# Kernel optimization log

Measured on AMD Instinct MI355X. Metric: run time of the kernel, lower is better.

The kernel has to match this reference:

```python
import jax, jax.numpy as jnp
import numpy as np

T, B, DIM, N = 2, 256, 512, 196


def setup_inputs() -> dict:
    key = jax.random.key(0)
    ks = jax.random.split(key, 6)
    scale_mem = (2.0 / (DIM + DIM)) ** 0.5      # GlorotNormal
    scale_cat = (2.0 / (2 * DIM + DIM)) ** 0.5
    scale_attn = (2.0 / (DIM + 1)) ** 0.5
    return {
        "memory": jax.random.normal(ks[0], (T, B, DIM), dtype=jnp.float32),
        "know": jax.random.normal(ks[1], (B, DIM, N), dtype=jnp.float32),
        "control": jax.random.normal(ks[2], (T, B, DIM), dtype=jnp.float32),
        "W_mem": jax.random.normal(ks[3], (DIM, DIM), dtype=jnp.float32) * scale_mem,
        "b_mem": jnp.zeros((DIM,), dtype=jnp.float32),
        "W_concat": jax.random.normal(ks[4], (2 * DIM, DIM), dtype=jnp.float32) * scale_cat,
        "b_concat": jnp.zeros((DIM,), dtype=jnp.float32),
        "W_attn": jax.random.normal(ks[5], (DIM, 1), dtype=jnp.float32) * scale_attn,
        "b_attn": jnp.zeros((1,), dtype=jnp.float32),
    }


def reference(memory, know, control, W_mem, b_mem, W_concat, b_concat, W_attn, b_attn):
    # mem = Dense(dim)(memory[-1]) -> [B, dim]
    mem = memory[-1] @ W_mem + b_mem
    # mem[..., None] * know -> [B, dim, N]; concat along channel axis -> [B, 2*dim, N]
    cat = jnp.concatenate([mem[:, :, None] * know, know], axis=1)
    # transpose to [B, N, 2*dim], Dense(dim) -> [B, N, dim]
    concat = jnp.swapaxes(cat, 1, 2) @ W_concat + b_concat
    # gate by control[-1] -> [B, N, dim]; Dense(1) + squeeze -> [B, N]
    attn = concat * control[-1][:, None, :]
    logits = jnp.squeeze(attn @ W_attn, -1) + b_attn[0]
    # softmax over N, then (faithfully) weighted sum over the dim axis -> [B, N]
    a = jax.nn.softmax(logits, axis=1)[:, None, :]  # [B, 1, N]
    read = jnp.sum(a * know, axis=1)  # [B, N]
    return read
```

## Files before the change

kernel.cpp:

```cpp
#include <hip/hip_runtime.h>
#include <cfloat>

#define BB   256
#define DIM  512
#define NN   196
#define BT   8
#define IT   32

__global__ __launch_bounds__(512, 4) void prep_kernel(
    const float* __restrict__ memory,
    const float* __restrict__ control,
    const float* __restrict__ W_mem,
    const float* __restrict__ b_mem,
    const float* __restrict__ W_concat,
    const float* __restrict__ W_attn,
    float* __restrict__ w_out)
{
    __shared__ float4 MU4[4][DIM];
    __shared__ float  buf[12288];

    const int tid = threadIdx.x;
    const int il  = tid & 31;
    const int kg  = tid >> 5;
    const int b0  = blockIdx.x * BT;
    const int i0  = blockIdx.y * IT;

    const float* mem_in = memory  + (size_t)BB * DIM;
    const float* ctl_in = control + (size_t)BB * DIM;

    {
        const float wa = W_attn[tid];
        #pragma unroll
        for (int p = 0; p < 4; ++p) {
            MU4[p][tid] = make_float4(
                mem_in[(size_t)(b0 + 2 * p)     * DIM + tid],
                ctl_in[(size_t)(b0 + 2 * p)     * DIM + tid] * wa,
                mem_in[(size_t)(b0 + 2 * p + 1) * DIM + tid],
                ctl_in[(size_t)(b0 + 2 * p + 1) * DIM + tid] * wa);
        }
    }

    float am[8] = {0,0,0,0,0,0,0,0};
    float a1[8] = {0,0,0,0,0,0,0,0};
    float a2[8] = {0,0,0,0,0,0,0,0};

    const int sr = tid >> 4;
    const int sc = tid & 15;
    float2* WT = (float2*)buf;

    float4 f1 = *(const float4*)&W_concat[(size_t)(i0 + sr) * DIM + sc * 4];
    float4 f2 = *(const float4*)&W_concat[(size_t)(DIM + i0 + sr) * DIM + sc * 4];
    float wmc[4], wmn[4];
    #pragma unroll
    for (int j = 0; j < 4; ++j)
        wmc[j] = W_mem[(size_t)(kg * 4 + j) * DIM + i0 + il];

    for (int kt = 0; kt < DIM; kt += 64) {
        __syncthreads();

        {
            const float* f1f = (const float*)&f1;
            const float* f2f = (const float*)&f2;
            #pragma unroll
            for (int j = 0; j < 4; ++j)
                WT[(sc * 4 + j) * 33 + sr] = make_float2(f1f[j], f2f[j]);
        }
        if (kt + 64 < DIM) {
            f1 = *(const float4*)&W_concat[(size_t)(i0 + sr) * DIM + kt + 64 + sc * 4];
            f2 = *(const float4*)&W_concat[(size_t)(DIM + i0 + sr) * DIM + kt + 64 + sc * 4];
        }
        __syncthreads();

        if (kt + 64 < DIM) {
            #pragma unroll
            for (int j = 0; j < 4; ++j)
                wmn[j] = W_mem[(size_t)(kt + 64 + kg * 4 + j) * DIM + i0 + il];
        }

        #pragma unroll
        for (int j = 0; j < 4; ++j) {
            const int kl = kg * 4 + j;
            const int k  = kt + kl;
            const float2 c = WT[kl * 33 + il];
            #pragma unroll
            for (int p = 0; p < 4; ++p) {
                const float4 mu = MU4[p][k];
                am[2 * p]     = fmaf(mu.x, wmc[j], am[2 * p]);
                a1[2 * p]     = fmaf(mu.y, c.x,    a1[2 * p]);
                a2[2 * p]     = fmaf(mu.y, c.y,    a2[2 * p]);
                am[2 * p + 1] = fmaf(mu.z, wmc[j], am[2 * p + 1]);
                a1[2 * p + 1] = fmaf(mu.w, c.x,    a1[2 * p + 1]);
                a2[2 * p + 1] = fmaf(mu.w, c.y,    a2[2 * p + 1]);
            }
        }
        #pragma unroll
        for (int j = 0; j < 4; ++j) wmc[j] = wmn[j];
    }

    __syncthreads();
    #pragma unroll
    for (int b = 0; b < 8; ++b) {
        const int row = (kg * 8 + b) * 32 + il;
        buf[row]        = am[b];
        buf[4096 + row] = a1[b];
        buf[8192 + row] = a2[b];
    }
    __syncthreads();
    if (tid < 256) {
        const int rb = tid >> 5, ri = tid & 31;
        float sm = 0.f, s1 = 0.f, s2 = 0.f;
        #pragma unroll
        for (int t = 0; t < 16; ++t) {
            const int row = (t * 8 + rb) * 32 + ri;
            sm += buf[row];
            s1 += buf[4096 + row];
            s2 += buf[8192 + row];
        }
        w_out[(size_t)(b0 + rb) * DIM + i0 + ri] =
            (sm + b_mem[i0 + ri]) * s1 + s2;
    }
}

__global__ __launch_bounds__(1024) void read_kernel(
    const float* __restrict__ know,
    const float* __restrict__ w,
    float* __restrict__ out)
{
    __shared__ float  w_s[DIM];
    __shared__ float4 part_lg[16][50];
    __shared__ float4 part_ks[16][50];
    __shared__ float  tmp[256];
    __shared__ float  bc[2];

    const int tx  = threadIdx.x;
    const int ty  = threadIdx.y;
    const int tid = ty * 64 + tx;
    const int b   = blockIdx.x;

    if (tid < DIM) w_s[tid] = w[(size_t)b * DIM + tid];
    __syncthreads();

    float4 lg = make_float4(0.f, 0.f, 0.f, 0.f);
    float4 ks = make_float4(0.f, 0.f, 0.f, 0.f);
    if (tx < 49) {
        const float4* kp = (const float4*)(know + (size_t)b * DIM * NN) + (size_t)(ty * 32) * 49 + tx;
        const float*  wp = w_s + ty * 32;
        #pragma unroll 8
        for (int dd = 0; dd < 32; ++dd) {
            const float4 kv = kp[(size_t)dd * 49];
            const float  wv = wp[dd];
            lg.x = fmaf(kv.x, wv, lg.x); lg.y = fmaf(kv.y, wv, lg.y);
            lg.z = fmaf(kv.z, wv, lg.z); lg.w = fmaf(kv.w, wv, lg.w);
            ks.x += kv.x; ks.y += kv.y; ks.z += kv.z; ks.w += kv.w;
        }
        part_lg[ty][tx] = lg;
        part_ks[ty][tx] = ks;
    }
    __syncthreads();

    float lgn = 0.f, ksn = 0.f;
    if (tid < NN) {
        const int ng = tid >> 2, j = tid & 3;
        #pragma unroll
        for (int t = 0; t < 16; ++t) {
            lgn += ((const float*)&part_lg[t][ng])[j];
            ksn += ((const float*)&part_ks[t][ng])[j];
        }
    }

    if (tid < 256) tmp[tid] = (tid < NN) ? lgn : -FLT_MAX;
    __syncthreads();
    if (tid < 64) {
        float m = fmaxf(fmaxf(tmp[tid], tmp[tid + 64]),
                        fmaxf(tmp[tid + 128], tmp[tid + 192]));
        #pragma unroll
        for (int o = 32; o; o >>= 1) m = fmaxf(m, __shfl_down(m, o));
        if (tid == 0) bc[0] = m;
    }
    __syncthreads();

    const float e = (tid < NN) ? __expf(lgn - bc[0]) : 0.f;
    if (tid < 256) tmp[tid] = e;
    __syncthreads();
    if (tid < 64) {
        float s = tmp[tid] + tmp[tid + 64] + tmp[tid + 128] + tmp[tid + 192];
        #pragma unroll
        for (int o = 32; o; o >>= 1) s += __shfl_down(s, o);
        if (tid == 0) bc[1] = s;
    }
    __syncthreads();

    if (tid < NN) out[(size_t)b * NN + tid] = e / bc[1] * ksn;
}

extern "C" void kernel_launch(void* const* d_in, const int* in_sizes, int n_in,
                              void* d_out, int out_size, void* d_ws, size_t ws_size,
                              hipStream_t stream) {
    const float* memory   = (const float*)d_in[0];
    const float* know     = (const float*)d_in[1];
    const float* control  = (const float*)d_in[2];
    const float* W_mem    = (const float*)d_in[3];
    const float* b_mem    = (const float*)d_in[4];
    const float* W_concat = (const float*)d_in[5];
    const float* W_attn   = (const float*)d_in[7];
    float* w_ws = (float*)d_ws;
    float* outp = (float*)d_out;

    prep_kernel<<<dim3(BB / BT, DIM / IT), dim3(512), 0, stream>>>(
        memory, control, W_mem, b_mem, W_concat, W_attn, w_ws);
    read_kernel<<<dim3(BB), dim3(64, 16), 0, stream>>>(know, w_ws, outp);
}
```

Baseline: 36.53 us.

## Widen prep kernel output tile to 64 columns for more register reuse

The prep kernel now computes 64 output columns per block instead of 32. Each thread keeps two sets of accumulators, so every shared-memory load of the memory/control values feeds twice as many FMAs. The grid is halved and launch bounds drop to 2 blocks per SM. Shared memory is merged into one buffer and the final cross-thread reduction is done in three passes to fit it, which adds extra barriers and lowers occupancy.

```diff
diff --git a/kernel.cpp b/kernel.cpp
--- a/kernel.cpp
+++ b/kernel.cpp
@@ -5,9 +5,9 @@
 #define DIM  512
 #define NN   196
 #define BT   8
-#define IT   32
-
-__global__ __launch_bounds__(512, 4) void prep_kernel(
+#define IT   64
+
+__global__ __launch_bounds__(512, 2) void prep_kernel(
     const float* __restrict__ memory,
     const float* __restrict__ control,
     const float* __restrict__ W_mem,
@@ -16,8 +16,9 @@
     const float* __restrict__ W_attn,
     float* __restrict__ w_out)
 {
-    __shared__ float4 MU4[4][DIM];
-    __shared__ float  buf[12288];
+    __shared__ float lds[16768];
+    float4* MU = (float4*)lds;
+    float2* WT = (float2*)(lds + 8192);
 
     const int tid = threadIdx.x;
     const int il  = tid & 31;
@@ -32,7 +33,7 @@
         const float wa = W_attn[tid];
         #pragma unroll
         for (int p = 0; p < 4; ++p) {
-            MU4[p][tid] = make_float4(
+            MU[p * 512 + tid] = make_float4(
                 mem_in[(size_t)(b0 + 2 * p)     * DIM + tid],
                 ctl_in[(size_t)(b0 + 2 * p)     * DIM + tid] * wa,
                 mem_in[(size_t)(b0 + 2 * p + 1) * DIM + tid],
@@ -40,85 +41,127 @@
         }
     }
 
-    float am[8] = {0,0,0,0,0,0,0,0};
-    float a1[8] = {0,0,0,0,0,0,0,0};
-    float a2[8] = {0,0,0,0,0,0,0,0};
-
     const int sr = tid >> 4;
     const int sc = tid & 15;
-    float2* WT = (float2*)buf;
-
-    float4 f1 = *(const float4*)&W_concat[(size_t)(i0 + sr) * DIM + sc * 4];
-    float4 f2 = *(const float4*)&W_concat[(size_t)(DIM + i0 + sr) * DIM + sc * 4];
-    float wmc[4], wmn[4];
-    #pragma unroll
-    for (int j = 0; j < 4; ++j)
-        wmc[j] = W_mem[(size_t)(kg * 4 + j) * DIM + i0 + il];
+    const float* w1l = W_concat + (size_t)(i0 + sr)            * DIM;
+    const float* w2l = W_concat + (size_t)(DIM + i0 + sr)      * DIM;
+    const float* w1h = W_concat + (size_t)(i0 + 32 + sr)       * DIM;
+    const float* w2h = W_concat + (size_t)(DIM + i0 + 32 + sr) * DIM;
+
+    float4 f1l = *(const float4*)(w1l + sc * 4);
+    float4 f2l = *(const float4*)(w2l + sc * 4);
+    float4 f1h = *(const float4*)(w1h + sc * 4);
+    float4 f2h = *(const float4*)(w2h + sc * 4);
+
+    float wmc[4][2], wmn[4][2];
+    #pragma unroll
+    for (int j = 0; j < 4; ++j) {
+        wmc[j][0] = W_mem[(size_t)(kg * 4 + j) * DIM + i0 + il];
+        wmc[j][1] = W_mem[(size_t)(kg * 4 + j) * DIM + i0 + 32 + il];
+    }
+
+    float am[8][2] = {}, a1[8][2] = {}, a2[8][2] = {};
 
     for (int kt = 0; kt < DIM; kt += 64) {
         __syncthreads();
 
         {
-            const float* f1f = (const float*)&f1;
-            const float* f2f = (const float*)&f2;
+            const float* pa = (const float*)&f1l;
+            const float* pb = (const float*)&f2l;
+            const float* pc = (const float*)&f1h;
+            const float* pd = (const float*)&f2h;
             #pragma unroll
-            for (int j = 0; j < 4; ++j)
-                WT[(sc * 4 + j) * 33 + sr] = make_float2(f1f[j], f2f[j]);
+            for (int cc = 0; cc < 4; ++cc) {
+                const int k = sc * 4 + cc;
+                WT[k * 67 + sr]      = make_float2(pa[cc], pb[cc]);
+                WT[k * 67 + 32 + sr] = make_float2(pc[cc], pd[cc]);
+            }
         }
         if (kt + 64 < DIM) {
-            f1 = *(const float4*)&W_concat[(size_t)(i0 + sr) * DIM + kt + 64 + sc * 4];
-            f2 = *(const float4*)&W_concat[(size_t)(DIM + i0 + sr) * DIM + kt + 64 + sc * 4];
+            f1l = *(const float4*)(w1l + kt + 64 + sc * 4);
+            f2l = *(const float4*)(w2l + kt + 64 + sc * 4);
+            f1h = *(const float4*)(w1h + kt + 64 + sc * 4);
+            f2h = *(const float4*)(w2h + kt + 64 + sc * 4);
         }
         __syncthreads();
 
         if (kt + 64 < DIM) {
             #pragma unroll
-            for (int j = 0; j < 4; ++j)
-                wmn[j] = W_mem[(size_t)(kt + 64 + kg * 4 + j) * DIM + i0 + il];
+            for (int j = 0; j < 4; ++j) {
+                wmn[j][0] = W_mem[(size_t)(kt + 64 + kg * 4 + j) * DIM + i0 + il];
+                wmn[j][1] = W_mem[(size_t)(kt + 64 + kg * 4 + j) * DIM + i0 + 32 + il];
+            }
         }
 
         #pragma unroll
         for (int j = 0; j < 4; ++j) {
             const int kl = kg * 4 + j;
             const int k  = kt + kl;
-            const float2 c = WT[kl * 33 + il];
+            const float2 cl = WT[kl * 67 + il];
+            const float2 ch = WT[kl * 67 + 32 + il];
             #pragma unroll
             for (int p = 0; p < 4; ++p) {
-                const float4 mu = MU4[p][k];
-                am[2 * p]     = fmaf(mu.x, wmc[j], am[2 * p]);
-                a1[2 * p]     = fmaf(mu.y, c.x,    a1[2 * p]);
-                a2[2 * p]     = fmaf(mu.y, c.y,    a2[2 * p]);
-                am[2 * p + 1] = fmaf(mu.z, wmc[j], am[2 * p + 1]);
-                a1[2 * p + 1] = fmaf(mu.w, c.x,    a1[2 * p + 1]);
-                a2[2 * p + 1] = fmaf(mu.w, c.y,    a2[2 * p + 1]);
+                const float4 mu = MU[p * 512 + k];
+                am[2*p][0]   = fmaf(mu.x, wmc[j][0], am[2*p][0]);
+                am[2*p][1]   = fmaf(mu.x, wmc[j][1], am[2*p][1]);
+                a1[2*p][0]   = fmaf(mu.y, cl.x, a1[2*p][0]);
+                a1[2*p][1]   = fmaf(mu.y, ch.x, a1[2*p][1]);
+                a2[2*p][0]   = fmaf(mu.y, cl.y, a2[2*p][0]);
+                a2[2*p][1]   = fmaf(mu.y, ch.y, a2[2*p][1]);
+                am[2*p+1][0] = fmaf(mu.z, wmc[j][0], am[2*p+1][0]);
+                am[2*p+1][1] = fmaf(mu.z, wmc[j][1], am[2*p+1][1]);
+                a1[2*p+1][0] = fmaf(mu.w, cl.x, a1[2*p+1][0]);
+                a1[2*p+1][1] = fmaf(mu.w, ch.x, a1[2*p+1][1]);
+                a2[2*p+1][0] = fmaf(mu.w, cl.y, a2[2*p+1][0]);
+                a2[2*p+1][1] = fmaf(mu.w, ch.y, a2[2*p+1][1]);
             }
         }
         #pragma unroll
-        for (int j = 0; j < 4; ++j) wmc[j] = wmn[j];
-    }
+        for (int j = 0; j < 4; ++j) {
+            wmc[j][0] = wmn[j][0];
+            wmc[j][1] = wmn[j][1];
+        }
+    }
+
+    const int rb  = tid >> 6;
+    const int ilo = tid & 63;
+    float sm, s1v, s2v;
 
     __syncthreads();
     #pragma unroll
     for (int b = 0; b < 8; ++b) {
-        const int row = (kg * 8 + b) * 32 + il;
-        buf[row]        = am[b];
-        buf[4096 + row] = a1[b];
-        buf[8192 + row] = a2[b];
-    }
-    __syncthreads();
-    if (tid < 256) {
-        const int rb = tid >> 5, ri = tid & 31;
-        float sm = 0.f, s1 = 0.f, s2 = 0.f;
-        #pragma unroll
-        for (int t = 0; t < 16; ++t) {
-            const int row = (t * 8 + rb) * 32 + ri;
-            sm += buf[row];
-            s1 += buf[4096 + row];
-            s2 += buf[8192 + row];
-        }
-        w_out[(size_t)(b0 + rb) * DIM + i0 + ri] =
-            (sm + b_mem[i0 + ri]) * s1 + s2;
-    }
+        lds[(kg * 8 + b) * 64 + il]      = am[b][0];
+        lds[(kg * 8 + b) * 64 + 32 + il] = am[b][1];
+    }
+    __syncthreads();
+    sm = 0.f;
+    #pragma unroll
+    for (int t = 0; t < 16; ++t) sm += lds[(t * 8 + rb) * 64 + ilo];
+
+    __syncthreads();
+    #pragma unroll
+    for (int b = 0; b < 8; ++b) {
+        lds[(kg * 8 + b) * 64 + il]      = a1[b][0];
+        lds[(kg * 8 + b) * 64 + 32 + il] = a1[b][1];
+    }
+    __syncthreads();
+    s1v = 0.f;
+    #pragma unroll
+    for (int t = 0; t < 16; ++t) s1v += lds[(t * 8 + rb) * 64 + ilo];
+
+    __syncthreads();
+    #pragma unroll
+    for (int b = 0; b < 8; ++b) {
+        lds[(kg * 8 + b) * 64 + il]      = a2[b][0];
+        lds[(kg * 8 + b) * 64 + 32 + il] = a2[b][1];
+    }
+    __syncthreads();
+    s2v = 0.f;
+    #pragma unroll
+    for (int t = 0; t < 16; ++t) s2v += lds[(t * 8 + rb) * 64 + ilo];
+
+    w_out[(size_t)(b0 + rb) * DIM + i0 + ilo] =
+        (sm + b_mem[i0 + ilo]) * s1v + s2v;
 }
 
 __global__ __launch_bounds__(1024) void read_kernel(
```

After: 36.70 us. Within noise of the previous version (+0.5%).

## Run prep GEMMs on bf16 MFMA with a separate conversion kernel

Applied to the files above, without the earlier changes.

Adds a conversion kernel that casts W_concat, a transposed W_mem, memory and the W_attn-scaled control rows to bf16 in workspace. A new prep kernel then computes the three small GEMMs with 16x16x32 bf16 MFMA instructions instead of scalar FP32 FMAs. This is meant to cut the FP32 FMA cost of the prep stage. In exchange it adds a kernel launch, an extra round trip through global memory and bf16 rounding error, and it keeps the old path as a fallback when the workspace is too small.

```diff
diff --git a/kernel.cpp b/kernel.cpp
--- a/kernel.cpp
+++ b/kernel.cpp
@@ -4,16 +4,144 @@
 #define BB   256
 #define DIM  512
 #define NN   196
-#define BT   8
-#define IT   32
-
-__global__ __launch_bounds__(512, 4) void prep_kernel(
-    const float* __restrict__ memory,
-    const float* __restrict__ control,
-    const float* __restrict__ W_mem,
+
+typedef __attribute__((ext_vector_type(8))) short bf16x8;
+typedef __attribute__((ext_vector_type(4))) float f32x4;
+
+__device__ __forceinline__ ushort f2bf(float x) {
+    unsigned u = __float_as_uint(x);
+    return (ushort)((u + 0x7FFFu + ((u >> 16) & 1u)) >> 16);
+}
+
+__global__ __launch_bounds__(256) void convert_kernel(
+    const float* __restrict__ memory, const float* __restrict__ control,
+    const float* __restrict__ W_mem, const float* __restrict__ W_concat,
+    const float* __restrict__ W_attn,
+    ushort* __restrict__ Wt,
+    ushort* __restrict__ mu)
+{
+    const int tid = threadIdx.x;
+    const int blk = blockIdx.x;
+
+    if (blk < 128) {
+        const float4* in4 = (const float4*)W_concat;
+        uint2* out = (uint2*)(Wt + (size_t)DIM * DIM);
+        #pragma unroll
+        for (int p = 0; p < 4; ++p) {
+            const int idx = blk * 1024 + p * 256 + tid;
+            const float4 q = in4[idx];
+            uint2 o;
+            o.x = (unsigned)f2bf(q.x) | ((unsigned)f2bf(q.y) << 16);
+            o.y = (unsigned)f2bf(q.z) | ((unsigned)f2bf(q.w) << 16);
+            out[idx] = o;
+        }
+    } else if (blk < 192) {
+        __shared__ float T[64][65];
+        const int t  = blk - 128;
+        const int tk = (t >> 3) * 64, ti = (t & 7) * 64;
+        const int r  = tid >> 2;
+        const int cb = (tid & 3) * 16;
+        #pragma unroll
+        for (int j = 0; j < 16; j += 4) {
+            const float4 q = *(const float4*)&W_mem[(size_t)(tk + r) * DIM + ti + cb + j];
+            T[r][cb + j + 0] = q.x; T[r][cb + j + 1] = q.y;
+            T[r][cb + j + 2] = q.z; T[r][cb + j + 3] = q.w;
+        }
+        __syncthreads();
+        const int ii = tid & 63;
+        const int kq = tid >> 6;
+        #pragma unroll
+        for (int kk = 0; kk < 16; kk += 2) {
+            const int k = kq * 16 + kk;
+            const unsigned v = (unsigned)f2bf(T[k][ii]) | ((unsigned)f2bf(T[k + 1][ii]) << 16);
+            *(unsigned*)&Wt[(size_t)(ti + ii) * DIM + tk + k] = v;
+        }
+    } else {
+        const float4* mem4 = (const float4*)(memory  + (size_t)BB * DIM);
+        const float4* ctl4 = (const float4*)(control + (size_t)BB * DIM);
+        const float4* wa4  = (const float4*)W_attn;
+        uint2* out = (uint2*)mu;
+        #pragma unroll
+        for (int p = 0; p < 4; ++p) {
+            const int idx = (blk - 192) * 1024 + p * 256 + tid;
+            const int sec = idx >> 15;
+            const int j   = idx & 32767;
+            float4 q = sec ? ctl4[j] : mem4[j];
+            if (sec) {
+                const float4 wa = wa4[j & 127];
+                q.x *= wa.x; q.y *= wa.y; q.z *= wa.z; q.w *= wa.w;
+            }
+            uint2 o;
+            o.x = (unsigned)f2bf(q.x) | ((unsigned)f2bf(q.y) << 16);
+            o.y = (unsigned)f2bf(q.z) | ((unsigned)f2bf(q.w) << 16);
+            out[(size_t)sec * 32768 + j] = o;
+        }
+    }
+}
+
+__global__ __launch_bounds__(128) void prep_mfma(
+    const ushort* __restrict__ Wt,
+    const ushort* __restrict__ mu,
     const float* __restrict__ b_mem,
-    const float* __restrict__ W_concat,
-    const float* __restrict__ W_attn,
+    float* __restrict__ w_out)
+{
+    __shared__ __align__(16) ushort mus[2][16][520];
+
+    const int tid = threadIdx.x;
+    const int wv  = tid >> 6;
+    const int l   = tid & 63;
+    const int b0  = blockIdx.x * 16;
+    const int i0  = blockIdx.y * 32;
+
+    #pragma unroll
+    for (int p = 0; p < 16; ++p) {
+        const int idx = p * 128 + tid;
+        const int a   = idx >> 10;
+        const int rb  = (idx >> 6) & 15;
+        const int kc  = (idx & 63) * 8;
+        *(uint4*)&mus[a][rb][kc] =
+            *(const uint4*)&mu[((size_t)a * BB + b0 + rb) * DIM + kc];
+    }
+    __syncthreads();
+
+    const int fr = l & 15;
+    const int fk = (l >> 4) * 8;
+
+    f32x4 accM = {0.f, 0.f, 0.f, 0.f};
+    f32x4 acc1 = {0.f, 0.f, 0.f, 0.f};
+    f32x4 acc2 = {0.f, 0.f, 0.f, 0.f};
+
+    const int ib = i0 + wv * 16 + fr;
+    const ushort* wm = Wt + ((size_t)0 * DIM + ib) * DIM;
+    const ushort* c1 = Wt + ((size_t)1 * DIM + ib) * DIM;
+    const ushort* c2 = Wt + ((size_t)2 * DIM + ib) * DIM;
+
+    #pragma unroll 4
+    for (int t = 0; t < 16; ++t) {
+        const int k = t * 32 + fk;
+        const bf16x8 am = *(const bf16x8*)&mus[0][fr][k];
+        const bf16x8 au = *(const bf16x8*)&mus[1][fr][k];
+        const bf16x8 bm = *(const bf16x8*)&wm[k];
+        const bf16x8 b1 = *(const bf16x8*)&c1[k];
+        const bf16x8 b2 = *(const bf16x8*)&c2[k];
+        accM = __builtin_amdgcn_mfma_f32_16x16x32_bf16(am, bm, accM, 0, 0, 0);
+        acc1 = __builtin_amdgcn_mfma_f32_16x16x32_bf16(au, b1, acc1, 0, 0, 0);
+        acc2 = __builtin_amdgcn_mfma_f32_16x16x32_bf16(au, b2, acc2, 0, 0, 0);
+    }
+
+    const float bmv = b_mem[ib];
+    const int rb0 = (l >> 4) * 4;
+    #pragma unroll
+    for (int r = 0; r < 4; ++r) {
+        w_out[(size_t)(b0 + rb0 + r) * DIM + ib] =
+            (accM[r] + bmv) * acc1[r] + acc2[r];
+    }
+}
+
+__global__ __launch_bounds__(512, 4) void prep_fallback(
+    const float* __restrict__ memory, const float* __restrict__ control,
+    const float* __restrict__ W_mem, const float* __restrict__ b_mem,
+    const float* __restrict__ W_concat, const float* __restrict__ W_attn,
     float* __restrict__ w_out)
 {
     __shared__ float4 MU4[4][DIM];
@@ -22,8 +150,8 @@
     const int tid = threadIdx.x;
     const int il  = tid & 31;
     const int kg  = tid >> 5;
-    const int b0  = blockIdx.x * BT;
-    const int i0  = blockIdx.y * IT;
+    const int b0  = blockIdx.x * 8;
+    const int i0  = blockIdx.y * 32;
 
     const float* mem_in = memory  + (size_t)BB * DIM;
     const float* ctl_in = control + (size_t)BB * DIM;
@@ -40,10 +168,7 @@
         }
     }
 
-    float am[8] = {0,0,0,0,0,0,0,0};
-    float a1[8] = {0,0,0,0,0,0,0,0};
-    float a2[8] = {0,0,0,0,0,0,0,0};
-
+    float am[8] = {}, a1[8] = {}, a2[8] = {};
     const int sr = tid >> 4;
     const int sc = tid & 15;
     float2* WT = (float2*)buf;
@@ -57,7 +182,6 @@
 
     for (int kt = 0; kt < DIM; kt += 64) {
         __syncthreads();
-
         {
             const float* f1f = (const float*)&f1;
             const float* f2f = (const float*)&f2;
@@ -70,13 +194,11 @@
             f2 = *(const float4*)&W_concat[(size_t)(DIM + i0 + sr) * DIM + kt + 64 + sc * 4];
         }
         __syncthreads();
-
         if (kt + 64 < DIM) {
             #pragma unroll
             for (int j = 0; j < 4; ++j)
                 wmn[j] = W_mem[(size_t)(kt + 64 + kg * 4 + j) * DIM + i0 + il];
         }
-
         #pragma unroll
         for (int j = 0; j < 4; ++j) {
             const int kl = kg * 4 + j;
@@ -84,13 +206,13 @@
             const float2 c = WT[kl * 33 + il];
             #pragma unroll
             for (int p = 0; p < 4; ++p) {
-                const float4 mu = MU4[p][k];
-                am[2 * p]     = fmaf(mu.x, wmc[j], am[2 * p]);
-                a1[2 * p]     = fmaf(mu.y, c.x,    a1[2 * p]);
-                a2[2 * p]     = fmaf(mu.y, c.y,    a2[2 * p]);
-                am[2 * p + 1] = fmaf(mu.z, wmc[j], am[2 * p + 1]);
-                a1[2 * p + 1] = fmaf(mu.w, c.x,    a1[2 * p + 1]);
-                a2[2 * p + 1] = fmaf(mu.w, c.y,    a2[2 * p + 1]);
+                const float4 muv = MU4[p][k];
+                am[2*p]   = fmaf(muv.x, wmc[j], am[2*p]);
+                a1[2*p]   = fmaf(muv.y, c.x,    a1[2*p]);
+                a2[2*p]   = fmaf(muv.y, c.y,    a2[2*p]);
+                am[2*p+1] = fmaf(muv.z, wmc[j], am[2*p+1]);
+                a1[2*p+1] = fmaf(muv.w, c.x,    a1[2*p+1]);
+                a2[2*p+1] = fmaf(muv.w, c.y,    a2[2*p+1]);
             }
         }
         #pragma unroll
@@ -203,10 +325,24 @@
     const float* b_mem    = (const float*)d_in[4];
     const float* W_concat = (const float*)d_in[5];
     const float* W_attn   = (const float*)d_in[7];
+    float* outp = (float*)d_out;
+
+    const size_t W_BYTES  = (size_t)BB * DIM * sizeof(float);
+    const size_t WT_BYTES = (size_t)3 * DIM * DIM * sizeof(ushort);
+    const size_t MU_BYTES = (size_t)2 * BB * DIM * sizeof(ushort);
+
     float* w_ws = (float*)d_ws;
-    float* outp = (float*)d_out;
-
-    prep_kernel<<<dim3(BB / BT, DIM / IT), dim3(512), 0, stream>>>(
-        memory, control, W_mem, b_mem, W_concat, W_attn, w_ws);
+
+    if (ws_size >= W_BYTES + WT_BYTES + MU_BYTES) {
+        ushort* Wt = (ushort*)((char*)d_ws + W_BYTES);
+        ushort* mu = (ushort*)((char*)d_ws + W_BYTES + WT_BYTES);
+        convert_kernel<<<dim3(256), dim3(256), 0, stream>>>(
+            memory, control, W_mem, W_concat, W_attn, Wt, mu);
+        prep_mfma<<<dim3(BB / 16, DIM / 32), dim3(128), 0, stream>>>(
+            Wt, mu, b_mem, w_ws);
+    } else {
+        prep_fallback<<<dim3(BB / 8, DIM / 32), dim3(512), 0, stream>>>(
+            memory, control, W_mem, b_mem, W_concat, W_attn, w_ws);
+    }
     read_kernel<<<dim3(BB), dim3(64, 16), 0, stream>>>(know, w_ws, outp);
 }
```

After: 33.12 us. -9.3%, faster.

## Fuse prep and read into one cooperative kernel with bf16 MFMA projections

Applied to the files above, without the earlier changes.

Replaces the two-kernel pipeline with a single cooperative-launch kernel. The first phase computes the per-batch weight vector using bf16 MFMA instructions over 256 blocks, then a grid-wide sync is followed by the softmax-weighted read phase. This removes a kernel launch boundary and moves the small GEMMs onto matrix cores, at the cost of bf16 rounding of the inputs and weights and the overhead of a grid barrier. A fallback to the old two-kernel path runs if the cooperative launch fails.

```diff
diff --git a/kernel.cpp b/kernel.cpp
--- a/kernel.cpp
+++ b/kernel.cpp
@@ -1,19 +1,204 @@
 #include <hip/hip_runtime.h>
+#include <hip/hip_cooperative_groups.h>
 #include <cfloat>
+
+namespace cg = cooperative_groups;
 
 #define BB   256
 #define DIM  512
 #define NN   196
-#define BT   8
-#define IT   32
-
-__global__ __launch_bounds__(512, 4) void prep_kernel(
+
+typedef __attribute__((ext_vector_type(8))) short bf16x8;
+typedef __attribute__((ext_vector_type(4))) float f32x4;
+
+__device__ __forceinline__ ushort f2bf(float x) {
+    unsigned u = __float_as_uint(x);
+    return (ushort)((u + 0x7FFFu + ((u >> 16) & 1u)) >> 16);
+}
+
+__device__ __forceinline__ bf16x8 pack8(float4 a, float4 b) {
+    union { bf16x8 v; ushort u[8]; } r;
+    r.u[0] = f2bf(a.x); r.u[1] = f2bf(a.y); r.u[2] = f2bf(a.z); r.u[3] = f2bf(a.w);
+    r.u[4] = f2bf(b.x); r.u[5] = f2bf(b.y); r.u[6] = f2bf(b.z); r.u[7] = f2bf(b.w);
+    return r.v;
+}
+
+__global__ __launch_bounds__(1024) void fused_kernel(
     const float* __restrict__ memory,
     const float* __restrict__ control,
     const float* __restrict__ W_mem,
     const float* __restrict__ b_mem,
     const float* __restrict__ W_concat,
     const float* __restrict__ W_attn,
+    const float* __restrict__ know,
+    float* __restrict__ w_ws,
+    float* __restrict__ out)
+{
+    __shared__ __align__(16) unsigned char smem[49152];
+
+    const int tid = threadIdx.x;
+    const int blk = blockIdx.x;
+
+    {
+        const int b0 = (blk & 15) * 16;
+        const int i0 = (blk >> 4) * 32;
+        ushort (*mus)[16][520] = (ushort (*)[16][520])smem;
+
+        const float* mem_in = memory  + (size_t)BB * DIM;
+        const float* ctl_in = control + (size_t)BB * DIM;
+
+        #pragma unroll
+        for (int p = 0; p < 4; ++p) {
+            const int idx = p * 1024 + tid;
+            const int a   = idx >> 11;
+            const int rb  = (idx >> 7) & 15;
+            const int k4  = idx & 127;
+            const float* src = a ? ctl_in : mem_in;
+            float4 q = *(const float4*)&src[(size_t)(b0 + rb) * DIM + k4 * 4];
+            if (a) {
+                const float4 wa = ((const float4*)W_attn)[k4];
+                q.x *= wa.x; q.y *= wa.y; q.z *= wa.z; q.w *= wa.w;
+            }
+            uint2 o;
+            o.x = (unsigned)f2bf(q.x) | ((unsigned)f2bf(q.y) << 16);
+            o.y = (unsigned)f2bf(q.z) | ((unsigned)f2bf(q.w) << 16);
+            *(uint2*)&mus[a][rb][k4 * 4] = o;
+        }
+        __syncthreads();
+
+        const int wv = tid >> 6;
+        const int l  = tid & 63;
+        const int s  = wv & 1;
+        const int c  = wv >> 1;
+        const int fr = l & 15;
+        const int fk = (l >> 4) * 8;
+        const int ib = i0 + s * 16 + fr;
+
+        f32x4 accM = {0.f,0.f,0.f,0.f}, acc1 = {0.f,0.f,0.f,0.f}, acc2 = {0.f,0.f,0.f,0.f};
+        const float* wmp = W_mem + ib;
+        const float* c1p = W_concat + (size_t)ib * DIM;
+        const float* c2p = W_concat + (size_t)(DIM + ib) * DIM;
+
+        #pragma unroll
+        for (int ts = 0; ts < 2; ++ts) {
+            const int k = c * 64 + ts * 32 + fk;
+            const bf16x8 am = *(const bf16x8*)&mus[0][fr][k];
+            const bf16x8 au = *(const bf16x8*)&mus[1][fr][k];
+            float wmv[8];
+            #pragma unroll
+            for (int j = 0; j < 8; ++j) wmv[j] = wmp[(size_t)(k + j) * DIM];
+            union { bf16x8 v; ushort u[8]; } bm;
+            #pragma unroll
+            for (int j = 0; j < 8; ++j) bm.u[j] = f2bf(wmv[j]);
+            const bf16x8 b1 = pack8(*(const float4*)&c1p[k], *(const float4*)&c1p[k + 4]);
+            const bf16x8 b2 = pack8(*(const float4*)&c2p[k], *(const float4*)&c2p[k + 4]);
+            accM = __builtin_amdgcn_mfma_f32_16x16x32_bf16(am, bm.v, accM, 0, 0, 0);
+            acc1 = __builtin_amdgcn_mfma_f32_16x16x32_bf16(au, b1,   acc1, 0, 0, 0);
+            acc2 = __builtin_amdgcn_mfma_f32_16x16x32_bf16(au, b2,   acc2, 0, 0, 0);
+        }
+
+        __syncthreads();
+        float* P = (float*)smem;
+        const int rb0 = (l >> 4) * 4;
+        #pragma unroll
+        for (int r = 0; r < 4; ++r) {
+            const int idx = (rb0 + r) * 16 + fr;
+            P[           wv * 256 + idx] = accM[r];
+            P[4096     + wv * 256 + idx] = acc1[r];
+            P[8192     + wv * 256 + idx] = acc2[r];
+        }
+        __syncthreads();
+        if (tid < 512) {
+            const int s2 = tid >> 8, idx = tid & 255;
+            float sm = 0.f, v1 = 0.f, v2 = 0.f;
+            #pragma unroll
+            for (int cc = 0; cc < 8; ++cc) {
+                const int w2 = cc * 2 + s2;
+                sm += P[       w2 * 256 + idx];
+                v1 += P[4096 + w2 * 256 + idx];
+                v2 += P[8192 + w2 * 256 + idx];
+            }
+            const int b = b0 + (idx >> 4);
+            const int i = i0 + s2 * 16 + (idx & 15);
+            w_ws[(size_t)b * DIM + i] = (sm + b_mem[i]) * v1 + v2;
+        }
+    }
+
+    __threadfence();
+    cg::this_grid().sync();
+
+    {
+        const int tx = tid & 63;
+        const int ty = tid >> 6;
+        const int b  = blk;
+        float*  w_s     = (float*)smem;
+        float4* part_lg = (float4*)(smem + 2048);
+        float4* part_ks = (float4*)(smem + 2048 + 12800);
+        float*  tmp     = (float*)(smem + 2048 + 25600);
+        float*  bc      = (float*)(smem + 2048 + 25600 + 1024);
+
+        if (tid < DIM) w_s[tid] = w_ws[(size_t)b * DIM + tid];
+        __syncthreads();
+
+        float4 lg = make_float4(0.f, 0.f, 0.f, 0.f);
+        float4 ks = make_float4(0.f, 0.f, 0.f, 0.f);
+        if (tx < 49) {
+            const float4* kp = (const float4*)(know + (size_t)b * DIM * NN)
+                             + (size_t)(ty * 32) * 49 + tx;
+            const float* wp = w_s + ty * 32;
+            #pragma unroll 8
+            for (int dd = 0; dd < 32; ++dd) {
+                const float4 kv = kp[(size_t)dd * 49];
+                const float  wv = wp[dd];
+                lg.x = fmaf(kv.x, wv, lg.x); lg.y = fmaf(kv.y, wv, lg.y);
+                lg.z = fmaf(kv.z, wv, lg.z); lg.w = fmaf(kv.w, wv, lg.w);
+                ks.x += kv.x; ks.y += kv.y; ks.z += kv.z; ks.w += kv.w;
+            }
+            part_lg[ty * 50 + tx] = lg;
+            part_ks[ty * 50 + tx] = ks;
+        }
+        __syncthreads();
+
+        float lgn = 0.f, ksn = 0.f;
+        if (tid < NN) {
+            const int ng = tid >> 2, j = tid & 3;
+            #pragma unroll
+            for (int t = 0; t < 16; ++t) {
+                lgn += ((const float*)&part_lg[t * 50 + ng])[j];
+                ksn += ((const float*)&part_ks[t * 50 + ng])[j];
+            }
+        }
+
+        if (tid < 256) tmp[tid] = (tid < NN) ? lgn : -FLT_MAX;
+        __syncthreads();
+        if (tid < 64) {
+            float m = fmaxf(fmaxf(tmp[tid], tmp[tid + 64]),
+                            fmaxf(tmp[tid + 128], tmp[tid + 192]));
+            #pragma unroll
+            for (int o = 32; o; o >>= 1) m = fmaxf(m, __shfl_down(m, o));
+            if (tid == 0) bc[0] = m;
+        }
+        __syncthreads();
+
+        const float e = (tid < NN) ? __expf(lgn - bc[0]) : 0.f;
+        if (tid < 256) tmp[tid] = e;
+        __syncthreads();
+        if (tid < 64) {
+            float s = tmp[tid] + tmp[tid + 64] + tmp[tid + 128] + tmp[tid + 192];
+            #pragma unroll
+            for (int o = 32; o; o >>= 1) s += __shfl_down(s, o);
+            if (tid == 0) bc[1] = s;
+        }
+        __syncthreads();
+
+        if (tid < NN) out[(size_t)b * NN + tid] = e / bc[1] * ksn;
+    }
+}
+
+__global__ __launch_bounds__(512, 4) void prep_fallback(
+    const float* __restrict__ memory, const float* __restrict__ control,
+    const float* __restrict__ W_mem, const float* __restrict__ b_mem,
+    const float* __restrict__ W_concat, const float* __restrict__ W_attn,
     float* __restrict__ w_out)
 {
     __shared__ float4 MU4[4][DIM];
@@ -22,8 +207,8 @@
     const int tid = threadIdx.x;
     const int il  = tid & 31;
     const int kg  = tid >> 5;
-    const int b0  = blockIdx.x * BT;
-    const int i0  = blockIdx.y * IT;
+    const int b0  = blockIdx.x * 8;
+    const int i0  = blockIdx.y * 32;
 
     const float* mem_in = memory  + (size_t)BB * DIM;
     const float* ctl_in = control + (size_t)BB * DIM;
@@ -40,10 +225,7 @@
         }
     }
 
-    float am[8] = {0,0,0,0,0,0,0,0};
-    float a1[8] = {0,0,0,0,0,0,0,0};
-    float a2[8] = {0,0,0,0,0,0,0,0};
-
+    float am[8] = {}, a1[8] = {}, a2[8] = {};
     const int sr = tid >> 4;
     const int sc = tid & 15;
     float2* WT = (float2*)buf;
@@ -57,7 +239,6 @@
 
     for (int kt = 0; kt < DIM; kt += 64) {
         __syncthreads();
-
         {
             const float* f1f = (const float*)&f1;
             const float* f2f = (const float*)&f2;
@@ -70,27 +251,25 @@
             f2 = *(const float4*)&W_concat[(size_t)(DIM + i0 + sr) * DIM + kt + 64 + sc * 4];
         }
         __syncthreads();
-
         if (kt + 64 < DIM) {
             #pragma unroll
             for (int j = 0; j < 4; ++j)
                 wmn[j] = W_mem[(size_t)(kt + 64 + kg * 4 + j) * DIM + i0 + il];
         }
-
         #pragma unroll
         for (int j = 0; j < 4; ++j) {
             const int kl = kg * 4 + j;
             const int k  = kt + kl;
-            const float2 c = WT[kl * 33 + il];
+            const float2 cc = WT[kl * 33 + il];
             #pragma unroll
             for (int p = 0; p < 4; ++p) {
-                const float4 mu = MU4[p][k];
-                am[2 * p]     = fmaf(mu.x, wmc[j], am[2 * p]);
-                a1[2 * p]     = fmaf(mu.y, c.x,    a1[2 * p]);
-                a2[2 * p]     = fmaf(mu.y, c.y,    a2[2 * p]);
-                am[2 * p + 1] = fmaf(mu.z, wmc[j], am[2 * p + 1]);
-                a1[2 * p + 1] = fmaf(mu.w, c.x,    a1[2 * p + 1]);
-                a2[2 * p + 1] = fmaf(mu.w, c.y,    a2[2 * p + 1]);
+                const float4 muv = MU4[p][k];
+                am[2*p]   = fmaf(muv.x, wmc[j], am[2*p]);
+                a1[2*p]   = fmaf(muv.y, cc.x,   a1[2*p]);
+                a2[2*p]   = fmaf(muv.y, cc.y,   a2[2*p]);
+                am[2*p+1] = fmaf(muv.z, wmc[j], am[2*p+1]);
+                a1[2*p+1] = fmaf(muv.w, cc.x,   a1[2*p+1]);
+                a2[2*p+1] = fmaf(muv.w, cc.y,   a2[2*p+1]);
             }
         }
         #pragma unroll
@@ -122,8 +301,7 @@
 }
 
 __global__ __launch_bounds__(1024) void read_kernel(
-    const float* __restrict__ know,
-    const float* __restrict__ w,
+    const float* __restrict__ know, const float* __restrict__ w,
     float* __restrict__ out)
 {
     __shared__ float  w_s[DIM];
@@ -206,7 +384,15 @@
     float* w_ws = (float*)d_ws;
     float* outp = (float*)d_out;
 
-    prep_kernel<<<dim3(BB / BT, DIM / IT), dim3(512), 0, stream>>>(
-        memory, control, W_mem, b_mem, W_concat, W_attn, w_ws);
-    read_kernel<<<dim3(BB), dim3(64, 16), 0, stream>>>(know, w_ws, outp);
-}
+    void* args[] = { (void*)&memory, (void*)&control, (void*)&W_mem,
+                     (void*)&b_mem, (void*)&W_concat, (void*)&W_attn,
+                     (void*)&know, (void*)&w_ws, (void*)&outp };
+    hipError_t err = hipLaunchCooperativeKernel(
+        (const void*)fused_kernel, dim3(BB), dim3(1024), args, 0, stream);
+
+    if (err != hipSuccess) {
+        prep_fallback<<<dim3(BB / 8, DIM / 32), dim3(512), 0, stream>>>(
+            memory, control, W_mem, b_mem, W_concat, W_attn, w_ws);
+        read_kernel<<<dim3(BB), dim3(64, 16), 0, stream>>>(know, w_ws, outp);
+    }
+}
```

Measured after the change: 118.8 us. 225% more time.
